# Performance work log

Hardware: AMD Instinct MI355X
Metric: run time of the kernel (lower is better)

## Reference

```python
import jax, jax.numpy as jnp
import numpy as np

PERMS = ((0, 1, 2, 3), (2, 1, 3, 0), (3, 1, 0, 2))


def setup_inputs() -> dict:
    key = jax.random.key(0)
    ks = jax.random.split(key, 10)
    N_n1, F = 50000, 128
    N_imp = 100000
    H = 512
    h = jax.random.normal(ks[0], (N_n1, F), dtype=jnp.float32)
    idx = jax.random.randint(ks[1], (N_imp, 4), 0, N_n1, dtype=jnp.int64)
    s = 0.05
    W1 = jax.random.normal(ks[2], (4 * F, H), dtype=jnp.float32) * s
    b1 = jax.random.normal(ks[3], (H,), dtype=jnp.float32) * s
    W2 = jax.random.normal(ks[4], (H, H), dtype=jnp.float32) * s
    b2 = jax.random.normal(ks[5], (H,), dtype=jnp.float32) * s
    W3 = jax.random.normal(ks[6], (H, H), dtype=jnp.float32) * s
    b3 = jax.random.normal(ks[7], (H,), dtype=jnp.float32) * s
    Wo = jax.random.normal(ks[8], (H, 2), dtype=jnp.float32) * s
    bo = jax.random.normal(ks[9], (2,), dtype=jnp.float32) * s
    return {"h": h, "idx": idx, "W1": W1, "b1": b1, "W2": W2, "b2": b2,
            "W3": W3, "b3": b3, "Wo": Wo, "bo": bo}


def reference(h, idx, W1, b1, W2, b2, W3, b3, Wo, bo):
    # Message passing: copy_u + mean over exactly one edge per relation == gather.
    hi = h[idx]  # [N, 4, F]
    N = hi.shape[0]
    # Stack the 3 permutations of the 4 neighbor features: [3, N, 4F]
    x = jnp.stack([hi[:, jnp.array(p), :].reshape(N, -1) for p in PERMS], axis=0)
    # Shared MLP (config = [512, relu] x 3), broadcast over permutation axis.
    x = jax.nn.relu(x @ W1 + b1)
    x = jax.nn.relu(x @ W2 + b2)
    x = jax.nn.relu(x @ W3 + b3)
    pooled = jnp.sum(x, axis=0)  # Janossy sum over permutations: [N, 512]
    return pooled @ Wo + bo  # [N, 2]
```

## Files before the change

kernel.cpp:

```cpp
#include <hip/hip_runtime.h>
#include <stdint.h>
#include <stddef.h>


typedef __attribute__((ext_vector_type(8))) short short8;
typedef __attribute__((ext_vector_type(4))) float f32x4;
typedef __attribute__((ext_vector_type(4))) float floatv4;
typedef __attribute__((ext_vector_type(8))) unsigned short ushort8;

#define GLOAD_LDS16(g, l)                                                      \
  __builtin_amdgcn_global_load_lds(                                            \
      (const __attribute__((address_space(1))) void*)(g),                      \
      (__attribute__((address_space(3))) void*)(l), 16, 0, 0)

__device__ __forceinline__ unsigned short f2bf(float f) {
  unsigned int u = __float_as_uint(f);
  u += 0x7fffu + ((u >> 16) & 1u);
  return (unsigned short)(u >> 16);
}
__device__ __forceinline__ float bf2f(unsigned short s) {
  return __uint_as_float(((unsigned int)s) << 16);
}

#define NNODES 100000
#define MTOT   300000
#define HD     512
#define NH     50000

__global__ __launch_bounds__(256) void prep_w(const float* __restrict__ W1,
                                              const float* __restrict__ W2,
                                              const float* __restrict__ W3,
                                              unsigned short* __restrict__ Wt) {
  int t = blockIdx.x * 256 + threadIdx.x;
  int layer = t >> 18;
  int r = t & 262143;
  int n = r >> 9, k = r & 511;
  const float* W = layer == 0 ? W1 : (layer == 1 ? W2 : W3);
  Wt[t] = f2bf(W[k * 512 + n]);
}

__global__ __launch_bounds__(256) void prep_hb(const float* __restrict__ h,
                                               unsigned short* __restrict__ hb) {
  int t = blockIdx.x * 256 + threadIdx.x;
  int v = t >> 4, c8 = (t & 15) * 8;
  const floatv4* hp = (const floatv4*)(h + (size_t)v * 128 + c8);
  floatv4 f0 = hp[0], f1 = hp[1];
  ushort8 o;
#pragma unroll
  for (int e = 0; e < 4; ++e) {
    o[e] = f2bf(f0[e]);
    o[4 + e] = f2bf(f1[e]);
  }
  *(ushort8*)(hb + (size_t)v * 128 + c8) = o;
}

__global__ __launch_bounds__(256) void init_out(float* __restrict__ out,
                                                const float* __restrict__ bo) {
  int t = blockIdx.x * 256 + threadIdx.x;
  if (t < 2 * NNODES) out[t] = bo[t & 1];
}

template <int GATHER, int FINAL>
__global__ __launch_bounds__(256, 2) void gemm_k(
    const unsigned short* __restrict__ A,
    const int* __restrict__ idx,
    const unsigned short* __restrict__ Wt,
    const float* __restrict__ bias,
    unsigned short* __restrict__ Xout,
    float* __restrict__ out, const float* __restrict__ Wo,
    int mchunk0) {
  __shared__ __align__(16) char smem[53248];
  char* sA = smem;
  char* sB = smem + 32768;
  int* sIdx = (int*)(smem + 49152);

  const int t = threadIdx.x;
  int bx = blockIdx.x;
  int xcd = bx & 7, tq = bx >> 3;
  int cbk = tq & 3;
  int rb = xcd + ((tq >> 2) << 3);
  int n0 = cbk * 128;
  int arow0 = rb * 256;
  int w = t >> 6, l = t & 63;
  int m16 = l & 15, q = l >> 4;

  if (GATHER) {
    int m = mchunk0 + arow0 + t;
    unsigned um = (unsigned)m;
    unsigned n = um / 3u;
    int p = (int)(um - n * 3u);
    if (n >= NNODES) n = 0;
    const unsigned pk0 = 0x320u, pk1 = 0x111u, pk2 = 0x032u, pk3 = 0x203u;
    int sh = p * 4;
    sIdx[t * 4 + 0] = idx[n * 4 + ((pk0 >> sh) & 0xFu)];
    sIdx[t * 4 + 1] = idx[n * 4 + ((pk1 >> sh) & 0xFu)];
    sIdx[t * 4 + 2] = idx[n * 4 + ((pk2 >> sh) & 0xFu)];
    sIdx[t * 4 + 3] = idx[n * 4 + ((pk3 >> sh) & 0xFu)];
    __syncthreads();
  }

  f32x4 acc[4][8];
#pragma unroll
  for (int i = 0; i < 4; ++i)
#pragma unroll
    for (int j = 0; j < 8; ++j) acc[i][j] = (f32x4){0.f, 0.f, 0.f, 0.f};

  for (int kt = 0; kt < 8; ++kt) {
    int kb = kt * 64;
    if (GATHER) {
      int jblk = kt >> 1;
      int inner = (kt & 1) * 64;
#pragma unroll
      for (int i = 0; i < 8; ++i) {
        int s = i * 256 + t;
        int r = s >> 3;
        int cl = (s & 7) ^ (r & 7);
        int src = sIdx[r * 4 + jblk];
        GLOAD_LDS16(A + (size_t)src * 128 + inner + cl * 8, sA + s * 16);
      }
    } else {
#pragma unroll
      for (int i = 0; i < 8; ++i) {
        int s = i * 256 + t;
        int r = s >> 3;
        int cl = (s & 7) ^ (r & 7);
        GLOAD_LDS16(A + (size_t)(arow0 + r) * HD + kb + cl * 8, sA + s * 16);
      }
    }
#pragma unroll
    for (int i = 0; i < 4; ++i) {
      int s = i * 256 + t;
      int r = s >> 3;
      int cl = (s & 7) ^ (r & 7);
      GLOAD_LDS16(Wt + (size_t)(n0 + r) * HD + kb + cl * 8, sB + s * 16);
    }
    __syncthreads();
#pragma unroll
    for (int ks = 0; ks < 2; ++ks) {
      short8 af[4], bfr[8];
      int cbp = ((ks << 2) + q) ^ (m16 & 7);
#pragma unroll
      for (int i = 0; i < 4; ++i) {
        int ra = w * 64 + i * 16 + m16;
        af[i] = *(const short8*)(sA + ra * 128 + cbp * 16);
      }
#pragma unroll
      for (int j = 0; j < 8; ++j) {
        int rn = j * 16 + m16;
        bfr[j] = *(const short8*)(sB + rn * 128 + cbp * 16);
      }
#pragma unroll
      for (int i = 0; i < 4; ++i)
#pragma unroll
        for (int j = 0; j < 8; ++j)
          acc[i][j] = __builtin_amdgcn_mfma_f32_16x16x32_bf16(af[i], bfr[j],
                                                              acc[i][j], 0, 0, 0);
    }
    __syncthreads();
  }

  unsigned short* L = (unsigned short*)smem;
  for (int ph = 0; ph < 2; ++ph) {
    __syncthreads();
    if ((w >> 1) == ph) {
      int wl = w & 1;
#pragma unroll
      for (int i = 0; i < 4; ++i)
#pragma unroll
        for (int j = 0; j < 8; ++j) {
          int coll = j * 16 + m16;
          float bv = bias[n0 + coll];
#pragma unroll
          for (int r = 0; r < 4; ++r) {
            int rowl = wl * 64 + i * 16 + q * 4 + r;
            float v = fmaxf(acc[i][j][r] + bv, 0.f);
            L[rowl * 136 + coll] = f2bf(v);
          }
        }
    }
    __syncthreads();
    if (!FINAL) {
#pragma unroll
      for (int v = 0; v < 8; ++v) {
        int chunk = v * 256 + t;
        int row = chunk >> 4, ch = chunk & 15;
        ushort8 val = *(const ushort8*)(L + row * 136 + ch * 8);
        *(ushort8*)(Xout + (size_t)(arow0 + ph * 128 + row) * HD + n0 + ch * 8) =
            val;
      }
    } else {
      int r2 = t >> 1, jo = t & 1;
      int grow = mchunk0 + arow0 + ph * 128 + r2;
      if (grow < MTOT) {
        const unsigned short* Lr = L + r2 * 136;
        float s = 0.f;
#pragma unroll
        for (int cc = 0; cc < 128; cc += 2) {
          unsigned int pair = *(const unsigned int*)(Lr + cc);
          s += bf2f((unsigned short)(pair & 0xffffu)) * Wo[(n0 + cc) * 2 + jo];
          s += bf2f((unsigned short)(pair >> 16)) * Wo[(n0 + cc + 1) * 2 + jo];
        }
        int node = grow / 3;
        atomicAdd(out + node * 2 + jo, s);
      }
    }
  }
}

extern "C" void kernel_launch(void* const* d_in, const int* in_sizes, int n_in,
                              void* d_out, int out_size, void* d_ws,
                              size_t ws_size, hipStream_t stream) {
  const float* h  = (const float*)d_in[0];
  const int*   ix = (const int*)d_in[1];
  const float* W1 = (const float*)d_in[2];
  const float* b1 = (const float*)d_in[3];
  const float* W2 = (const float*)d_in[4];
  const float* b2 = (const float*)d_in[5];
  const float* W3 = (const float*)d_in[6];
  const float* b3 = (const float*)d_in[7];
  const float* Wo = (const float*)d_in[8];
  const float* bo = (const float*)d_in[9];
  float* out = (float*)d_out;

  unsigned short* ws = (unsigned short*)d_ws;
  unsigned short* Wt = ws;
  unsigned short* hb = Wt + 786432;
  unsigned short* bufs = hb + 6400000;
  const size_t baseBytes = (786432ull + 6400000ull) * 2;

  size_t avail = ws_size > baseBytes ? ws_size - baseBytes : 0;
  size_t ncap = avail / (2ull * 3 * HD * sizeof(unsigned short));
  size_t nc = (ncap / 2048) * 2048;
  if (nc > 32768) nc = 32768;
  if (nc == 0) nc = 2048;
  unsigned short* X1 = bufs;
  unsigned short* X2 = X1 + nc * 3 * HD;

  prep_w<<<3072, 256, 0, stream>>>(W1, W2, W3, Wt);
  prep_hb<<<NH * 16 / 256, 256, 0, stream>>>(h, hb);
  init_out<<<(2 * NNODES + 255) / 256, 256, 0, stream>>>(out, bo);

  for (size_t n0c = 0; n0c < NNODES; n0c += nc) {
    size_t remn = (size_t)NNODES - n0c;
    size_t ncp = remn < nc ? ((remn + 2047) / 2048) * 2048 : nc;
    int rows = (int)(ncp * 3);
    int RB = rows / 256;
    int m0 = (int)(3 * n0c);
    gemm_k<1, 0><<<RB * 4, 256, 0, stream>>>(hb, ix, Wt, b1, X1, nullptr,
                                             nullptr, m0);
    gemm_k<0, 0><<<RB * 4, 256, 0, stream>>>(X1, nullptr, Wt + 262144, b2, X2,
                                             nullptr, nullptr, m0);
    gemm_k<0, 1><<<RB * 4, 256, 0, stream>>>(X2, nullptr, Wt + 524288, b3,
                                             nullptr, out, Wo, m0);
  }
}
```

Measured before the change: 759.0 us.

## Switch GEMM to 128x128 tiles with 32x32x16 MFMA and higher occupancy

Shrinks the block tile from 256x128 to 128x128 with a 2x2 wave layout, each wave computing 64x64 using 32x32x16 bf16 MFMA instead of 16x16x32. This halves LDS use and accumulator registers, which allows four blocks per CU instead of two, and removes the two-phase epilogue. The cost is lower arithmetic intensity per block, since the weight tile is reloaded for twice as many row blocks, and more blocks are launched.

Result: faster. 700.9 us (-7.6%).

```diff
diff --git a/kernel.cpp b/kernel.cpp
--- a/kernel.cpp
+++ b/kernel.cpp
@@ -4,7 +4,7 @@
 
 
 typedef __attribute__((ext_vector_type(8))) short short8;
-typedef __attribute__((ext_vector_type(4))) float f32x4;
+typedef __attribute__((ext_vector_type(16))) float f32x16;
 typedef __attribute__((ext_vector_type(4))) float floatv4;
 typedef __attribute__((ext_vector_type(8))) unsigned short ushort8;
 
@@ -61,7 +61,7 @@
 }
 
 template <int GATHER, int FINAL>
-__global__ __launch_bounds__(256, 2) void gemm_k(
+__global__ __launch_bounds__(256, 4) void gemm_k(
     const unsigned short* __restrict__ A,
     const int* __restrict__ idx,
     const unsigned short* __restrict__ Wt,
@@ -69,10 +69,10 @@
     unsigned short* __restrict__ Xout,
     float* __restrict__ out, const float* __restrict__ Wo,
     int mchunk0) {
-  __shared__ __align__(16) char smem[53248];
+  __shared__ __align__(16) char smem[36864];
   char* sA = smem;
-  char* sB = smem + 32768;
-  int* sIdx = (int*)(smem + 49152);
+  char* sB = smem + 16384;
+  int* sIdx = (int*)(smem + 32768);
 
   const int t = threadIdx.x;
   int bx = blockIdx.x;
@@ -80,30 +80,35 @@
   int cbk = tq & 3;
   int rb = xcd + ((tq >> 2) << 3);
   int n0 = cbk * 128;
-  int arow0 = rb * 256;
+  int arow0 = rb * 128;
   int w = t >> 6, l = t & 63;
-  int m16 = l & 15, q = l >> 4;
+  int wm = (w >> 1) * 64, wn = (w & 1) * 64;
+  int m32 = l & 31, half = l >> 5;
 
   if (GATHER) {
-    int m = mchunk0 + arow0 + t;
-    unsigned um = (unsigned)m;
-    unsigned n = um / 3u;
-    int p = (int)(um - n * 3u);
-    if (n >= NNODES) n = 0;
-    const unsigned pk0 = 0x320u, pk1 = 0x111u, pk2 = 0x032u, pk3 = 0x203u;
-    int sh = p * 4;
-    sIdx[t * 4 + 0] = idx[n * 4 + ((pk0 >> sh) & 0xFu)];
-    sIdx[t * 4 + 1] = idx[n * 4 + ((pk1 >> sh) & 0xFu)];
-    sIdx[t * 4 + 2] = idx[n * 4 + ((pk2 >> sh) & 0xFu)];
-    sIdx[t * 4 + 3] = idx[n * 4 + ((pk3 >> sh) & 0xFu)];
+    if (t < 128) {
+      int m = mchunk0 + arow0 + t;
+      unsigned um = (unsigned)m;
+      unsigned n = um / 3u;
+      int p = (int)(um - n * 3u);
+      if (n >= NNODES) n = 0;
+      const unsigned pk0 = 0x320u, pk1 = 0x111u, pk2 = 0x032u, pk3 = 0x203u;
+      int sh = p * 4;
+      sIdx[t * 4 + 0] = idx[n * 4 + ((pk0 >> sh) & 0xFu)];
+      sIdx[t * 4 + 1] = idx[n * 4 + ((pk1 >> sh) & 0xFu)];
+      sIdx[t * 4 + 2] = idx[n * 4 + ((pk2 >> sh) & 0xFu)];
+      sIdx[t * 4 + 3] = idx[n * 4 + ((pk3 >> sh) & 0xFu)];
+    }
     __syncthreads();
   }
 
-  f32x4 acc[4][8];
-#pragma unroll
-  for (int i = 0; i < 4; ++i)
-#pragma unroll
-    for (int j = 0; j < 8; ++j) acc[i][j] = (f32x4){0.f, 0.f, 0.f, 0.f};
+  f32x16 acc[2][2];
+#pragma unroll
+  for (int i = 0; i < 2; ++i)
+#pragma unroll
+    for (int j = 0; j < 2; ++j)
+#pragma unroll
+      for (int r = 0; r < 16; ++r) acc[i][j][r] = 0.f;
 
   for (int kt = 0; kt < 8; ++kt) {
     int kb = kt * 64;
@@ -111,7 +116,7 @@
       int jblk = kt >> 1;
       int inner = (kt & 1) * 64;
 #pragma unroll
-      for (int i = 0; i < 8; ++i) {
+      for (int i = 0; i < 4; ++i) {
         int s = i * 256 + t;
         int r = s >> 3;
         int cl = (s & 7) ^ (r & 7);
@@ -120,7 +125,7 @@
       }
     } else {
 #pragma unroll
-      for (int i = 0; i < 8; ++i) {
+      for (int i = 0; i < 4; ++i) {
         int s = i * 256 + t;
         int r = s >> 3;
         int cl = (s & 7) ^ (r & 7);
@@ -136,73 +141,63 @@
     }
     __syncthreads();
 #pragma unroll
-    for (int ks = 0; ks < 2; ++ks) {
-      short8 af[4], bfr[8];
-      int cbp = ((ks << 2) + q) ^ (m16 & 7);
-#pragma unroll
-      for (int i = 0; i < 4; ++i) {
-        int ra = w * 64 + i * 16 + m16;
-        af[i] = *(const short8*)(sA + ra * 128 + cbp * 16);
-      }
-#pragma unroll
-      for (int j = 0; j < 8; ++j) {
-        int rn = j * 16 + m16;
-        bfr[j] = *(const short8*)(sB + rn * 128 + cbp * 16);
-      }
-#pragma unroll
-      for (int i = 0; i < 4; ++i)
-#pragma unroll
-        for (int j = 0; j < 8; ++j)
-          acc[i][j] = __builtin_amdgcn_mfma_f32_16x16x32_bf16(af[i], bfr[j],
+    for (int ks = 0; ks < 4; ++ks) {
+      short8 af[2], bfr[2];
+      int cb = ((ks << 1) + half) ^ (m32 & 7);
+#pragma unroll
+      for (int i = 0; i < 2; ++i)
+        af[i] = *(const short8*)(sA + (wm + i * 32 + m32) * 128 + cb * 16);
+#pragma unroll
+      for (int j = 0; j < 2; ++j)
+        bfr[j] = *(const short8*)(sB + (wn + j * 32 + m32) * 128 + cb * 16);
+#pragma unroll
+      for (int i = 0; i < 2; ++i)
+#pragma unroll
+        for (int j = 0; j < 2; ++j)
+          acc[i][j] = __builtin_amdgcn_mfma_f32_32x32x16_bf16(af[i], bfr[j],
                                                               acc[i][j], 0, 0, 0);
     }
     __syncthreads();
   }
 
   unsigned short* L = (unsigned short*)smem;
-  for (int ph = 0; ph < 2; ++ph) {
-    __syncthreads();
-    if ((w >> 1) == ph) {
-      int wl = w & 1;
-#pragma unroll
-      for (int i = 0; i < 4; ++i)
-#pragma unroll
-        for (int j = 0; j < 8; ++j) {
-          int coll = j * 16 + m16;
-          float bv = bias[n0 + coll];
-#pragma unroll
-          for (int r = 0; r < 4; ++r) {
-            int rowl = wl * 64 + i * 16 + q * 4 + r;
-            float v = fmaxf(acc[i][j][r] + bv, 0.f);
-            L[rowl * 136 + coll] = f2bf(v);
-          }
-        }
-    }
-    __syncthreads();
-    if (!FINAL) {
-#pragma unroll
-      for (int v = 0; v < 8; ++v) {
-        int chunk = v * 256 + t;
-        int row = chunk >> 4, ch = chunk & 15;
-        ushort8 val = *(const ushort8*)(L + row * 136 + ch * 8);
-        *(ushort8*)(Xout + (size_t)(arow0 + ph * 128 + row) * HD + n0 + ch * 8) =
-            val;
-      }
-    } else {
-      int r2 = t >> 1, jo = t & 1;
-      int grow = mchunk0 + arow0 + ph * 128 + r2;
-      if (grow < MTOT) {
-        const unsigned short* Lr = L + r2 * 136;
-        float s = 0.f;
-#pragma unroll
-        for (int cc = 0; cc < 128; cc += 2) {
-          unsigned int pair = *(const unsigned int*)(Lr + cc);
-          s += bf2f((unsigned short)(pair & 0xffffu)) * Wo[(n0 + cc) * 2 + jo];
-          s += bf2f((unsigned short)(pair >> 16)) * Wo[(n0 + cc + 1) * 2 + jo];
-        }
-        int node = grow / 3;
-        atomicAdd(out + node * 2 + jo, s);
-      }
+#pragma unroll
+  for (int i = 0; i < 2; ++i)
+#pragma unroll
+    for (int j = 0; j < 2; ++j) {
+      int coll = wn + j * 32 + m32;
+      float bv = bias[n0 + coll];
+#pragma unroll
+      for (int r = 0; r < 16; ++r) {
+        int rowl = wm + i * 32 + (r & 3) + 8 * (r >> 2) + 4 * half;
+        float v = fmaxf(acc[i][j][r] + bv, 0.f);
+        L[rowl * 136 + coll] = f2bf(v);
+      }
+    }
+  __syncthreads();
+
+  if (!FINAL) {
+#pragma unroll
+    for (int v = 0; v < 8; ++v) {
+      int chunk = v * 256 + t;
+      int row = chunk >> 4, ch = chunk & 15;
+      ushort8 val = *(const ushort8*)(L + row * 136 + ch * 8);
+      *(ushort8*)(Xout + (size_t)(arow0 + row) * HD + n0 + ch * 8) = val;
+    }
+  } else {
+    int r2 = t >> 1, jo = t & 1;
+    int grow = mchunk0 + arow0 + r2;
+    if (grow < MTOT) {
+      const unsigned short* Lr = L + r2 * 136;
+      float s = 0.f;
+#pragma unroll
+      for (int cc = 0; cc < 128; cc += 2) {
+        unsigned int pair = *(const unsigned int*)(Lr + cc);
+        s += bf2f((unsigned short)(pair & 0xffffu)) * Wo[(n0 + cc) * 2 + jo];
+        s += bf2f((unsigned short)(pair >> 16)) * Wo[(n0 + cc + 1) * 2 + jo];
+      }
+      int node = grow / 3;
+      atomicAdd(out + node * 2 + jo, s);
     }
   }
 }
@@ -244,7 +239,7 @@
     size_t remn = (size_t)NNODES - n0c;
     size_t ncp = remn < nc ? ((remn + 2047) / 2048) * 2048 : nc;
     int rows = (int)(ncp * 3);
-    int RB = rows / 256;
+    int RB = rows / 128;
     int m0 = (int)(3 * n0c);
     gemm_k<1, 0><<<RB * 4, 256, 0, stream>>>(hb, ix, Wt, b1, X1, nullptr,
                                              nullptr, m0);
```
